# Performance work log

Measured on AMD Instinct MI355X. Metric: run time of the kernel, lower is better.

## Reference

```python
import jax, jax.numpy as jnp
import numpy as np

MAX_SLOTS = 8192


def _compress_lowest_importance_pair(x):
    """Vectorized version of the per-batch python loop: merge the adjacent pair
    with the lowest summed L2-norm into one averaged slot. [B,S,d] -> [B,S-1,d]."""
    B, S, d = x.shape
    imp = jnp.linalg.norm(x, axis=-1)              # [B, S]
    pair_scores = imp[:, :-1] + imp[:, 1:]          # [B, S-1]
    p = jnp.argmin(pair_scores, axis=1)             # [B] merge index per row
    idx = jnp.arange(S - 1)                         # output slot positions
    # gather: out[j] = x[j] for j<=p, x[j+1] for j>p
    g = idx[None, :] + (idx[None, :] > p[:, None]).astype(idx.dtype)  # [B, S-1]
    out = jnp.take_along_axis(x, g[:, :, None], axis=1)               # [B, S-1, d]
    left = jnp.take_along_axis(x, p[:, None, None], axis=1)           # [B, 1, d]
    right = jnp.take_along_axis(x, (p + 1)[:, None, None], axis=1)    # [B, 1, d]
    merged = 0.5 * (left + right)
    # overwrite position p with the merged slot
    out = jnp.where(idx[None, :, None] == p[:, None, None], merged, out)
    return out


def _compress_oldest_pair(x):
    merged = 0.5 * (x[:, :1, :] + x[:, 1:2, :])
    return jnp.concatenate([merged, x[:, 2:, :]], axis=1)


def setup_inputs() -> dict:
    key = jax.random.key(0)
    k1, k2 = jax.random.split(key)
    bank_states = jax.random.normal(k1, (16, 8192, 512), dtype=jnp.float32)
    refresh_states = jax.random.normal(k2, (16, 32, 512), dtype=jnp.float32)
    return {"bank_states": bank_states, "refresh_states": refresh_states}


def reference(bank_states, refresh_states):
    # write(): refresh_states.detach(); sizes here take the concat+compress path
    refresh = jax.lax.stop_gradient(refresh_states)
    updated = jnp.concatenate([bank_states, refresh], axis=1)  # [B, S_bank+S_ref, d]
    # shapes are static, so this python while unrolls a fixed number of steps
    while updated.shape[1] > MAX_SLOTS:
        if updated.shape[1] <= 2:
            updated = _compress_oldest_pair(updated)
        else:
            updated = _compress_lowest_importance_pair(updated)
    return updated
```

## Files before the change

### kernel.cpp

```cpp
#include <hip/hip_runtime.h>
#include <cstdint>
#include <cstddef>

#define B_DIM  16
#define S_BANK 8192
#define S_REF  32
#define S_TOT  8224
#define NMERGE 32
#define D      512
#define NCH    129

typedef float vfloat4 __attribute__((ext_vector_type(4)));
typedef unsigned long long u64;
#define DEADPK 0xFFFFFFFFFFFFFFFFULL

__device__ __forceinline__ int d_lo(double d){ union{double d; int i[2];}u; u.d=d; return u.i[0]; }
__device__ __forceinline__ int d_hi(double d){ union{double d; int i[2];}u; u.d=d; return u.i[1]; }
__device__ __forceinline__ double d_mk(int hi,int lo){ union{double d; int i[2];}u; u.i[0]=lo;u.i[1]=hi; return u.d; }
__device__ __forceinline__ int u_lo(u64 v){ return (int)(v & 0xFFFFFFFFULL); }
__device__ __forceinline__ int u_hi(u64 v){ return (int)(v >> 32); }
__device__ __forceinline__ u64 u_mk(int hi,int lo){ return ((u64)(unsigned)hi << 32) | (u64)(unsigned)lo; }
__device__ __forceinline__ u64 d_bits(double d){ union{double d; u64 u;}x; x.d=d; return x.u; }

__device__ __forceinline__ u64 pack_score(double s, int j) {
// ... 54 lines not shown
}
__device__ __forceinline__ double sum_wave(double v) {
    sum_level<0x111>(v); sum_level<0x112>(v); sum_level<0x114>(v);
    sum_level<0x118>(v); sum_level<0x142>(v); sum_level<0x143>(v);
    int lo = __builtin_amdgcn_readlane(d_lo(v), 63);
    int hi = __builtin_amdgcn_readlane(d_hi(v), 63);
    return d_mk(hi, lo);
}

__global__ __launch_bounds__(256) void norms_kernel(const float* __restrict__ bank,
                                                    const float* __restrict__ refresh,
                                                    double* __restrict__ norms) {
    int gw_lin = (int)((blockIdx.x * 256 + threadIdx.x) >> 6);
    int gw   = B_DIM * S_TOT - 1 - gw_lin;
    int lane = threadIdx.x & 63;
    int b = gw / S_TOT;
    int s = gw - b * S_TOT;
    const float4* src = (const float4*)(s < S_BANK
        ? bank    + ((size_t)b * S_BANK + s) * D
        : refresh + ((size_t)b * S_REF + (s - S_BANK)) * D);
    float4 f0 = src[lane];
    float4 f1 = src[lane + 64];
    double acc = 0.0;
    acc += (double)f0.x * f0.x + (double)f0.y * f0.y + (double)f0.z * f0.z + (double)f0.w * f0.w;
    acc += (double)f1.x * f1.x + (double)f1.y * f1.y + (double)f1.z * f1.z + (double)f1.w * f1.w;
    acc = sum_wave(acc);
    if (lane == 0) norms[gw] = sqrt(acc);
}

__global__ __launch_bounds__(256) void chunkmin_kernel(const double* __restrict__ norms,
                                                       u64* __restrict__ c_pk_g) {
    int w    = (int)((blockIdx.x * 256 + threadIdx.x) >> 6);
    int lane = threadIdx.x & 63;
    if (w >= B_DIM * NCH) return;
    int b = w / NCH;
    int c = w - b * NCH;
    int j = c * 64 + lane;
    u64 pk = DEADPK;
    if (j <= S_TOT - 2) {
        double a = norms[b * S_TOT + j];
        double d = norms[b * S_TOT + j + 1];
        pk = pack_score(a + d, j);
    }
    pk = lexmin_wave_u64(pk);
    if (lane == 0) c_pk_g[b * NCH + c] = pk;
}

__device__ __forceinline__ const float* slot_gptr(int id, int b,
        const float* bank, const float* refresh) {
    return (id < S_BANK) ? bank    + ((size_t)b * S_BANK + id) * D
                         : refresh + ((size_t)b * S_REF + (id - S_BANK)) * D;
}

struct FastLds {
    u64 pref[192];
    u64 suf[192];
};
struct FallLds {
    unsigned short s_next[S_TOT];
    float          s_mvec[NMERGE][D];
    unsigned short s_mpos[NMERGE];
    unsigned short s_dead[NMERGE];
};
union MergeLds { FastLds fast; FallLds fall; };

__global__ __launch_bounds__(256) void merge_kernel(const float* __restrict__ bank,
        const float* __restrict__ refresh, const double* __restrict__ norms,
        const u64* __restrict__ c_pk_g,
        float* __restrict__ merged, unsigned short* __restrict__ idx_out) {
    __shared__ double  s_imp[S_TOT];
    __shared__ u64     c_pk[NCH];
    __shared__ MergeLds u;
    __shared__ int     rec_L[NMERGE], rec_R[NMERGE];
    __shared__ u64     rec_chosen[NMERGE];
    __shared__ u64     s_PL, s_SR;
    __shared__ int     s_flag;

    const int t    = threadIdx.x;
    const int b    = blockIdx.x;
    const int lane = t & 63;
    const int wid  = t >> 6;
    const double INF = __builtin_inf();

    if (t < NCH) c_pk[t] = c_pk_g[b * NCH + t];
    __syncthreads();

    u64 pk_min0;
    {
        u64 a = c_pk[lane];
        u64 bq = c_pk[lane + 64];
        u64 c = (lane == 0) ? c_pk[128] : DEADPK;
        u64 m = (a < bq) ? a : bq;
        m = (m < c) ? m : c;
        pk_min0 = lexmin_wave_u64(m);
    }
    const int p0 = (int)(pk_min0 & 0x3FFFULL);

    const int cmid = p0 >> 6;
    int wsx = cmid - 1;
    if (wsx < 0) wsx = 0;
    if (wsx > NCH - 3) wsx = NCH - 3;
    const int ws  = wsx;
    const int wlo = ws * 64;

    float4 m0r, m1r;

    int do_fall = 1;
    {
        FastLds& F = u.fast;

        for (int j = t; j < 194; j += 256) {
            int g = wlo + j;
            if (g < S_TOT) s_imp[g] = norms[b * S_TOT + g];
        }
        __syncthreads();

        if (wid == 0) {
            const float4* gA = (const float4*)slot_gptr(p0, b, bank, refresh);
            const float4* gB = (const float4*)slot_gptr(p0 + 1, b, bank, refresh);
            float4 a0 = gA[2 * lane], a1 = gA[2 * lane + 1];
            float4 b0 = gB[2 * lane], b1 = gB[2 * lane + 1];
            int q;
            q = (p0 - 1 >= 0) ? p0 - 1 : 0;
            const float4* gq = (const float4*)slot_gptr(q, b, bank, refresh);
            float4 cL0 = gq[2 * lane], cL1 = gq[2 * lane + 1];
            q = (p0 + 2 <= S_TOT - 1) ? p0 + 2 : S_TOT - 1;
            gq = (const float4*)slot_gptr(q, b, bank, refresh);
            float4 cR0 = gq[2 * lane], cR1 = gq[2 * lane + 1];
            q = (p0 - 2 >= 0) ? p0 - 2 : 0;
            gq = (const float4*)slot_gptr(q, b, bank, refresh);
            float4 fL0 = gq[2 * lane], fL1 = gq[2 * lane + 1];
            q = (p0 + 3 <= S_TOT - 1) ? p0 + 3 : S_TOT - 1;
            gq = (const float4*)slot_gptr(q, b, bank, refresh);
            float4 fR0 = gq[2 * lane], fR1 = gq[2 * lane + 1];

            m0r.x = 0.5f * (a0.x + b0.x); m0r.y = 0.5f * (a0.y + b0.y);
            m0r.z = 0.5f * (a0.z + b0.z); m0r.w = 0.5f * (a0.w + b0.w);
            m1r.x = 0.5f * (a1.x + b1.x); m1r.y = 0.5f * (a1.y + b1.y);
            m1r.z = 0.5f * (a1.z + b1.z); m1r.w = 0.5f * (a1.w + b1.w);
            double ss = 0.0;
            ss += (double)m0r.x * m0r.x + (double)m0r.y * m0r.y + (double)m0r.z * m0r.z + (double)m0r.w * m0r.w;
            ss += (double)m1r.x * m1r.x + (double)m1r.y * m1r.y + (double)m1r.z * m1r.z + (double)m1r.w * m1r.w;
            double nrm = sqrt(sum_wave(ss));
            int L = p0, R = p0 + 1;
            if (t == 0) { rec_L[0] = L; rec_R[0] = R; rec_chosen[0] = pk_min0; }

            for (int step = 1; step < NMERGE; ++step) {
                const int cl = L - 1, cr = R + 1;
                const bool hasL = (cl >= 0);
                const bool hasR = (cr < S_TOT);
                const double il = hasL ? s_imp[cl] : INF;
                const double ir = hasR ? s_imp[cr] : INF;
                const u64 pkL = hasL ? pack_score(il + nrm, cl) : DEADPK;
                const u64 pkR = hasR ? pack_score(nrm + ir, L)  : DEADPK;
                const bool goL = (pkL < pkR);
                const u64 chosen = goL ? pkL : pkR;
                float4 a0s, a1s, b0s, b1s;
                if (goL) { a0s = cL0; a1s = cL1; b0s = m0r; b1s = m1r; }
                else     { a0s = m0r; a1s = m1r; b0s = cR0; b1s = cR1; }
                m0r.x = 0.5f * (a0s.x + b0s.x); m0r.y = 0.5f * (a0s.y + b0s.y);
                m0r.z = 0.5f * (a0s.z + b0s.z); m0r.w = 0.5f * (a0s.w + b0s.w);
                m1r.x = 0.5f * (a1s.x + b1s.x); m1r.y = 0.5f * (a1s.y + b1s.y);
                m1r.z = 0.5f * (a1s.z + b1s.z); m1r.w = 0.5f * (a1s.w + b1s.w);
                if (goL) {
                    L = cl;
                    cL0 = fL0; cL1 = fL1;
                    int nq = (L - 2 >= 0) ? L - 2 : 0;
                    const float4* gp = (const float4*)slot_gptr(nq, b, bank, refresh);
                    fL0 = gp[2 * lane]; fL1 = gp[2 * lane + 1];
                } else {
                    R = cr;
                    cR0 = fR0; cR1 = fR1;
                    int nq = (R + 2 <= S_TOT - 1) ? R + 2 : S_TOT - 1;
                    const float4* gp = (const float4*)slot_gptr(nq, b, bank, refresh);
                    fR0 = gp[2 * lane]; fR1 = gp[2 * lane + 1];
                }
                double ss2 = 0.0;
                ss2 += (double)m0r.x * m0r.x + (double)m0r.y * m0r.y + (double)m0r.z * m0r.z + (double)m0r.w * m0r.w;
                ss2 += (double)m1r.x * m1r.x + (double)m1r.y * m1r.y + (double)m1r.z * m1r.z + (double)m1r.w * m1r.w;
                nrm = sqrt(sum_wave(ss2));
                if (t == 0) { rec_L[step] = L; rec_R[step] = R; rec_chosen[step] = chosen; }
            }
        } else {
            int c = ws + (wid - 1);
            int idx = c * 64 + lane;
            u64 pk0 = (idx <= S_TOT - 2) ? pack_score(s_imp[idx] + s_imp[idx + 1], idx)
                                         : DEADPK;
            F.pref[idx - wlo] = scan_min_incl(pk0);
            F.suf[idx - wlo]  = scan_min_suffix(pk0, lane);
            if (wid == 1) {
                u64 x0 = (lane < ws) ? c_pk[lane] : DEADPK;
                u64 x1 = (lane + 64 < ws) ? c_pk[lane + 64] : DEADPK;
                u64 pl = (x0 < x1) ? x0 : x1;
                pl = lexmin_wave_u64(pl);
                if (lane == 0) s_PL = pl;
            }
            if (wid == 2) {
                u64 y0 = (lane > ws + 2) ? c_pk[lane] : DEADPK;
                u64 y1 = (lane + 64 > ws + 2) ? c_pk[lane + 64] : DEADPK;
                u64 y2 = (lane == 0 && 128 > ws + 2) ? c_pk[128] : DEADPK;
                u64 sr = (y0 < y1) ? y0 : y1;
                sr = (sr < y2) ? sr : y2;
                sr = lexmin_wave_u64(sr);
                if (lane == 0) s_SR = sr;
            }
        }
        __syncthreads();

        if (wid == 0) {
            u64 cf0 = F.pref[63], cf1 = F.pref[127];
            u64 sf1 = F.suf[64],  sf2 = F.suf[128];
            u64 PL = s_PL, SR = s_SR;
            bool ok = true;
            if (lane >= 1 && lane < NMERGE) {
                int Lp = rec_L[lane - 1], Rp = rec_R[lane - 1];
                int q1 = Lp - 2 - wlo;
                u64 ol = DEADPK;
                if (q1 >= 0) {
                    ol = F.pref[q1];
                    int r1 = q1 >> 6;
                    if (r1 >= 1 && cf0 < ol) ol = cf0;
                    if (r1 >= 2 && cf1 < ol) ol = cf1;
                }
                if (PL < ol) ol = PL;
                int q2 = Rp + 1 - wlo;
                u64 orr = F.suf[q2];
                int r2 = q2 >> 6;
                if (r2 <= 0 && sf1 < orr) orr = sf1;
                if (r2 <= 1 && sf2 < orr) orr = sf2;
                if (SR < orr) orr = SR;
                u64 O = (ol < orr) ? ol : orr;
                ok = rec_chosen[lane] < O;
            }
            if (lane == 0) ok = ok && (rec_R[NMERGE - 1] - rec_L[NMERGE - 1] == NMERGE);
            unsigned long long bad = __ballot(!ok);
            if (lane == 0) s_flag = (bad != 0ULL) ? 1 : 0;
        }
        __syncthreads();

        if (s_flag == 0) {
            if (wid == 0) {
                float4* dst = (float4*)(merged + ((size_t)b * NMERGE + (NMERGE - 1)) * D);
                dst[2 * lane] = m0r; dst[2 * lane + 1] = m1r;
            }
            const int Ls = rec_L[NMERGE - 1], Rs = rec_R[NMERGE - 1];
            for (int j = t; j < S_TOT; j += 256) {
                if (j < Ls)       idx_out[b * S_BANK + j] = (unsigned short)j;
                else if (j == Ls) idx_out[b * S_BANK + j] = (unsigned short)(S_TOT + NMERGE - 1);
                else if (j > Rs)  idx_out[b * S_BANK + j - NMERGE] = (unsigned short)j;
            }
            do_fall = 0;
        }
    }

    if (do_fall) {
        FallLds& G = u.fall;
        for (int j = t; j < S_TOT; j += 256)
            s_imp[j] = norms[b * S_TOT + j];
        for (int j = t; j < S_TOT; j += 256)
            G.s_next[j] = (unsigned short)((j + 1 < S_TOT) ? (j + 1) : 0xFFFF);
        __syncthreads();

        if (wid == 0) {
            u64 cv0 = c_pk[lane];
            u64 cv1 = c_pk[lane + 64];
            u64 cv2 = (lane == 0) ? c_pk[128] : DEADPK;

            int mpos_reg = -1;
            int prev_p = -1, prev_pv = -1, prev_nk = -1;
            int pvok = 0, nkok = 0;
            float4 mm0, mm1, pva0, pva1, pnk0, pnk1;

            for (int step = 0; step < NMERGE; ++step) {
                u64 m = (cv0 < cv1) ? cv0 : cv1;
                m = (m < cv2) ? m : cv2;
                m = lexmin_wave_u64(m);
                const int p = (int)(m & 0x3FFFULL);

                const bool hitA = pvok && (p == prev_pv);
                const bool hitB = nkok && (p == prev_p);

                int k, nk;
                float4 a0, a1, b0, b1;
                if (hitA) {
                    k = prev_p; nk = prev_nk;
                    a0 = pva0; a1 = pva1; b0 = mm0; b1 = mm1;
                } else if (hitB) {
                    k = prev_nk; nk = G.s_next[k];
                    a0 = mm0; a1 = mm1; b0 = pnk0; b1 = pnk1;
                } else {
                    k = G.s_next[p]; nk = G.s_next[k];
                    unsigned long long bA = __ballot((lane < step) && (mpos_reg == p));
                    const int ia = bA ? (S_TOT + 63 - __clzll(bA)) : p;
                    unsigned long long bB = __ballot((lane < step) && (mpos_reg == k));
                    const int ib = bB ? (S_TOT + 63 - __clzll(bB)) : k;
                    if (ia < S_TOT) { const float4* g = (const float4*)slot_gptr(ia, b, bank, refresh);
                                      a0 = g[2 * lane]; a1 = g[2 * lane + 1]; }
                    else            { const float4* g = (const float4*)&G.s_mvec[ia - S_TOT][0];
                                      a0 = g[2 * lane]; a1 = g[2 * lane + 1]; }
                    if (ib < S_TOT) { const float4* g = (const float4*)slot_gptr(ib, b, bank, refresh);
                                      b0 = g[2 * lane]; b1 = g[2 * lane + 1]; }
                    else            { const float4* g = (const float4*)&G.s_mvec[ib - S_TOT][0];
                                      b0 = g[2 * lane]; b1 = g[2 * lane + 1]; }
                }

                int pv;
                if (hitB) {
                    pv = prev_pv;
                } else {
                    int jq = p - 1 - lane;
                    bool plive = (jq >= 0) && (s_imp[jq] < 1e300);
                    unsigned long long pb = __ballot(plive);
                    pv = pb ? (p - __ffsll((unsigned long long)pb)) : -1;
                }

                const double imp_nk = s_imp[(nk != 0xFFFF) ? nk : 0];
                const double imp_pv = s_imp[(pv >= 0) ? pv : 0];
                const int chp = p >> 6, chk = k >> 6;
                const int chv = (pv >= 0) ? (pv >> 6) : -1;
                const int csB = (chk != chp) ? chk : -1;
                const int csC = (chv >= 0 && chv != chp && chv != chk) ? chv : -1;
                const int jjA = chp * 64 + lane;
                const bool validA = (jjA < S_TOT) && (jjA != k);
                const int rawNxtA = validA ? (int)G.s_next[jjA] : 0xFFFF;
                const double impA = validA ? s_imp[jjA] : INF;
                const int nxtA = (jjA == p) ? nk : rawNxtA;
                const double impNxtA = (nxtA != 0xFFFF) ? s_imp[nxtA] : INF;

                float4 m0, m1;
                m0.x = 0.5f * (a0.x + b0.x); m0.y = 0.5f * (a0.y + b0.y);
                m0.z = 0.5f * (a0.z + b0.z); m0.w = 0.5f * (a0.w + b0.w);
                m1.x = 0.5f * (a1.x + b1.x); m1.y = 0.5f * (a1.y + b1.y);
                m1.z = 0.5f * (a1.z + b1.z); m1.w = 0.5f * (a1.w + b1.w);
                {
                    float4* dst = (float4*)&G.s_mvec[step][0];
                    dst[2 * lane] = m0; dst[2 * lane + 1] = m1;
                }
                if (lane == step) mpos_reg = p;

                if (step + 1 < NMERGE) {
                    prev_p = p; prev_pv = pv; prev_nk = nk;
                    mm0 = m0; mm1 = m1;
                    pvok = (pv >= 0); nkok = (nk != 0xFFFF);
                    unsigned long long bpv = __ballot((lane <= step) && (mpos_reg == pv));
                    const int ipv = bpv ? (S_TOT + 63 - __clzll(bpv)) : pv;
                    unsigned long long bnk = __ballot((lane <= step) && (mpos_reg == nk));
                    const int ink = bnk ? (S_TOT + 63 - __clzll(bnk)) : nk;
                    if (pvok) {
                        if (ipv < S_TOT) { const float4* g = (const float4*)slot_gptr(ipv, b, bank, refresh);
                                           pva0 = g[2 * lane]; pva1 = g[2 * lane + 1]; }
                        else             { const float4* g = (const float4*)&G.s_mvec[ipv - S_TOT][0];
                                           pva0 = g[2 * lane]; pva1 = g[2 * lane + 1]; }
                    }
                    if (nkok) {
                        if (ink < S_TOT) { const float4* g = (const float4*)slot_gptr(ink, b, bank, refresh);
                                           pnk0 = g[2 * lane]; pnk1 = g[2 * lane + 1]; }
                        else             { const float4* g = (const float4*)&G.s_mvec[ink - S_TOT][0];
                                           pnk0 = g[2 * lane]; pnk1 = g[2 * lane + 1]; }
                    }
                }

                double ss = 0.0;
                ss += (double)m0.x * m0.x + (double)m0.y * m0.y + (double)m0.z * m0.z + (double)m0.w * m0.w;
                ss += (double)m1.x * m1.x + (double)m1.y * m1.y + (double)m1.z * m1.z + (double)m1.w * m1.w;
                const double nrm = sqrt(sum_wave(ss));

                if (lane == 0) {
                    G.s_next[p]    = (unsigned short)nk;
                    s_imp[k]       = INF;
                    s_imp[p]       = nrm;
                    G.s_mpos[step] = (unsigned short)p;
                    G.s_dead[step] = (unsigned short)k;
                }

                {
                    u64 sc = DEADPK;
                    if (validA && nxtA != 0xFFFF) {
                        double a0d = (jjA == p) ? nrm : impA;
                        if (a0d < 1e300) {
                            double a1d = (nxtA == p) ? nrm : impNxtA;
                            sc = pack_score(a0d + a1d, jjA);
                        }
                    }
                    sc = lexmin_wave_u64(sc);
                    if (chp < 64)       { if (lane == chp)      cv0 = sc; }
                    else if (chp < 128) { if (lane == chp - 64) cv1 = sc; }
                    else                { if (lane == 0)        cv2 = sc; }
                }
                if (csB >= 0) {
                    int jj = csB * 64 + lane;
                    u64 sc = DEADPK;
                    if (jj < S_TOT && jj != k) {
                        int nxt = (int)G.s_next[jj];
                        if (nxt != 0xFFFF) {
                            double a0d = s_imp[jj];
                            if (a0d < 1e300) sc = pack_score(a0d + s_imp[nxt], jj);
                        }
                    }
                    sc = lexmin_wave_u64(sc);
                    if (csB < 64)       { if (lane == csB)      cv0 = sc; }
                    else if (csB < 128) { if (lane == csB - 64) cv1 = sc; }
                    else                { if (lane == 0)        cv2 = sc; }
                }
                if (csC >= 0) {
                    int jj = csC * 64 + lane;
                    u64 sc = DEADPK;
                    if (jj < S_TOT && jj != k) {
                        int nxt = (int)G.s_next[jj];
                        if (nxt != 0xFFFF) {
                            double a0d = s_imp[jj];
                            if (a0d < 1e300) sc = pack_score(a0d + s_imp[nxt], jj);
                        }
                    }
                    sc = lexmin_wave_u64(sc);
                    if (csC < 64)       { if (lane == csC)      cv0 = sc; }
                    else if (csC < 128) { if (lane == csC - 64) cv1 = sc; }
                    else                { if (lane == 0)        cv2 = sc; }
                }
            }
        }
        __syncthreads();

        {
            const float4* src = (const float4*)&G.s_mvec[0][0];
            float4* dst = (float4*)(merged + (size_t)b * NMERGE * D);
            for (int i = t; i < NMERGE * D / 4; i += 256) dst[i] = src[i];
        }
        for (int j = t; j < S_TOT; j += 256) G.s_next[j] = 0xFFFF;
        __syncthreads();
        if (t == 0)
            for (int m2 = 0; m2 < NMERGE; ++m2) G.s_next[G.s_mpos[m2]] = (unsigned short)m2;
        __syncthreads();
        for (int j = t; j < S_TOT; j += 256) {
            if (s_imp[j] < 1e300) {
                int r = j;
                #pragma unroll
                for (int m2 = 0; m2 < NMERGE; ++m2) r -= (G.s_dead[m2] < j) ? 1 : 0;
                unsigned short lut = G.s_next[j];
                idx_out[b * S_BANK + r] = (lut != 0xFFFF) ? (unsigned short)(S_TOT + lut)
                                                          : (unsigned short)j;
            }
        }
    }
}

__global__ __launch_bounds__(256) void gather_kernel(const vfloat4* __restrict__ bank,
        const vfloat4* __restrict__ refresh, const vfloat4* __restrict__ merged,
        const unsigned short* __restrict__ idx, vfloat4* __restrict__ out) {
    size_t tid = (size_t)blockIdx.x * 256 + threadIdx.x;
    int slot = (int)(tid >> 7);
    int c    = (int)(tid & 127);
    int b    = slot >> 13;
    int src  = idx[slot];
    const vfloat4* sp;
    if (src < S_BANK)     sp = bank    + ((size_t)b * S_BANK + src) * (D / 4);
    else if (src < S_TOT) sp = refresh + ((size_t)b * S_REF + (src - S_BANK)) * (D / 4);
    else                  sp = merged  + ((size_t)b * NMERGE + (src - S_TOT)) * (D / 4);
    vfloat4 v = sp[c];
    __builtin_nontemporal_store(v, &out[tid]);
}

extern "C" void kernel_launch(void* const* d_in, const int* in_sizes, int n_in,
                              void* d_out, int out_size, void* d_ws, size_t ws_size,
                              hipStream_t stream) {
    const float* bank    = (const float*)d_in[0];
    const float* refresh = (const float*)d_in[1];

    double*         norms  = (double*)d_ws;
    float*          merged = (float*)((char*)d_ws + (size_t)B_DIM * S_TOT * sizeof(double));
    unsigned short* idx    = (unsigned short*)((char*)merged + (size_t)B_DIM * NMERGE * D * sizeof(float));
    u64*            c_pk_g = (u64*)((char*)idx + (size_t)B_DIM * S_BANK * sizeof(unsigned short));
    float*          out    = (float*)d_out;

    norms_kernel<<<(B_DIM * S_TOT) / 4, 256, 0, stream>>>(bank, refresh, norms);
    chunkmin_kernel<<<(B_DIM * NCH * 64 + 255) / 256, 256, 0, stream>>>(norms, c_pk_g);
    merge_kernel<<<B_DIM, 256, 0, stream>>>(bank, refresh, norms, c_pk_g, merged, idx);
    gather_kernel<<<(size_t)B_DIM * S_BANK * (D / 4) / 256, 256, 0, stream>>>(
        (const vfloat4*)bank, (const vfloat4*)refresh, (const vfloat4*)merged, idx, (vfloat4*)out);
}
```

Before: 144.9 us.

## Fuse merge and gather into one kernel with per-batch fallback kernel

Merges the greedy merge step and the output gather into one launch. Extra blocks copy the bulk rows, whose position is known from the first merge index p0, while 16 blocks run the local merge chain and write the window around p0 directly. This removes the idx indirection and the separate merged buffer. A flag per batch triggers a separate fallback kernel that recomputes everything for that batch when the local fast path fails verification. The cost is an extra launch and redundant work per bulk block, since each one recomputes p0 from the chunk minima.

```diff
diff --git a/kernel.cpp b/kernel.cpp
--- a/kernel.cpp
+++ b/kernel.cpp
@@ -130,35 +130,55 @@
                          : refresh + ((size_t)b * S_REF + (id - S_BANK)) * D;
 }
 
-struct FastLds {
-    u64 pref[192];
-    u64 suf[192];
-};
-struct FallLds {
-    unsigned short s_next[S_TOT];
-    float          s_mvec[NMERGE][D];
-    unsigned short s_mpos[NMERGE];
-    unsigned short s_dead[NMERGE];
-};
-union MergeLds { FastLds fast; FallLds fall; };
-
-__global__ __launch_bounds__(256) void merge_kernel(const float* __restrict__ bank,
+#define NBULK (B_DIM * 4096)
+
+__global__ __launch_bounds__(256) void fused_kernel(const float* __restrict__ bank,
         const float* __restrict__ refresh, const double* __restrict__ norms,
-        const u64* __restrict__ c_pk_g,
-        float* __restrict__ merged, unsigned short* __restrict__ idx_out) {
-    __shared__ double  s_imp[S_TOT];
-    __shared__ u64     c_pk[NCH];
-    __shared__ MergeLds u;
-    __shared__ int     rec_L[NMERGE], rec_R[NMERGE];
-    __shared__ u64     rec_chosen[NMERGE];
-    __shared__ u64     s_PL, s_SR;
-    __shared__ int     s_flag;
+        const u64* __restrict__ c_pk_g, int* __restrict__ flag_g,
+        vfloat4* __restrict__ out) {
+    __shared__ double s_wimp[194];
+    __shared__ u64    c_pk[NCH];
+    __shared__ u64    pref[192], suf[192];
+    __shared__ int    rec_L[NMERGE], rec_R[NMERGE];
+    __shared__ u64    rec_chosen[NMERGE];
+    __shared__ u64    s_PL, s_SR;
+    __shared__ int    s_flag;
+    __shared__ int    sh_p0;
 
     const int t    = threadIdx.x;
-    const int b    = blockIdx.x;
     const int lane = t & 63;
     const int wid  = t >> 6;
     const double INF = __builtin_inf();
+
+    if (blockIdx.x >= 16) {
+        int e  = blockIdx.x - 16;
+        int b  = e >> 12;
+        int pr = (e & 4095) << 1;
+        if (wid == 0) {
+            u64 a  = (lane < NCH) ? c_pk_g[b * NCH + lane] : DEADPK;
+            u64 b2 = (lane + 64 < NCH) ? c_pk_g[b * NCH + lane + 64] : DEADPK;
+            u64 m = (a < b2) ? a : b2;
+            u64 c2 = (lane == 0) ? c_pk_g[b * NCH + 128] : DEADPK;
+            m = (m < c2) ? m : c2;
+            m = lexmin_wave_u64(m);
+            if (lane == 0) sh_p0 = (int)(m & 0x3FFFULL);
+        }
+        __syncthreads();
+        const int p0 = sh_p0;
+        int r = pr + (t >> 7);
+        int c = t & 127;
+        int s = -1;
+        if (r < p0 - 31)      s = r;
+        else if (r > p0)      s = r + 32;
+        if (s >= 0) {
+            const vfloat4* sp = (const vfloat4*)slot_gptr(s, b, bank, refresh);
+            vfloat4 v = sp[c];
+            __builtin_nontemporal_store(v, &out[((size_t)b * S_BANK + r) * (D / 4) + c]);
+        }
+        return;
+    }
+
+    const int b = blockIdx.x;
 
     if (t < NCH) c_pk[t] = c_pk_g[b * NCH + t];
     __syncthreads();
@@ -181,361 +201,381 @@
     const int ws  = wsx;
     const int wlo = ws * 64;
 
+    for (int j = t; j < 194; j += 256) {
+        int g = wlo + j;
+        if (g < S_TOT) s_wimp[j] = norms[b * S_TOT + g];
+    }
+    __syncthreads();
+
     float4 m0r, m1r;
 
-    int do_fall = 1;
-    {
-        FastLds& F = u.fast;
-
-        for (int j = t; j < 194; j += 256) {
-            int g = wlo + j;
-            if (g < S_TOT) s_imp[g] = norms[b * S_TOT + g];
-        }
-        __syncthreads();
-
-        if (wid == 0) {
-            const float4* gA = (const float4*)slot_gptr(p0, b, bank, refresh);
-            const float4* gB = (const float4*)slot_gptr(p0 + 1, b, bank, refresh);
-            float4 a0 = gA[2 * lane], a1 = gA[2 * lane + 1];
-            float4 b0 = gB[2 * lane], b1 = gB[2 * lane + 1];
-            int q;
-            q = (p0 - 1 >= 0) ? p0 - 1 : 0;
-            const float4* gq = (const float4*)slot_gptr(q, b, bank, refresh);
-            float4 cL0 = gq[2 * lane], cL1 = gq[2 * lane + 1];
-            q = (p0 + 2 <= S_TOT - 1) ? p0 + 2 : S_TOT - 1;
-            gq = (const float4*)slot_gptr(q, b, bank, refresh);
-            float4 cR0 = gq[2 * lane], cR1 = gq[2 * lane + 1];
-            q = (p0 - 2 >= 0) ? p0 - 2 : 0;
-            gq = (const float4*)slot_gptr(q, b, bank, refresh);
-            float4 fL0 = gq[2 * lane], fL1 = gq[2 * lane + 1];
-            q = (p0 + 3 <= S_TOT - 1) ? p0 + 3 : S_TOT - 1;
-            gq = (const float4*)slot_gptr(q, b, bank, refresh);
-            float4 fR0 = gq[2 * lane], fR1 = gq[2 * lane + 1];
-
-            m0r.x = 0.5f * (a0.x + b0.x); m0r.y = 0.5f * (a0.y + b0.y);
-            m0r.z = 0.5f * (a0.z + b0.z); m0r.w = 0.5f * (a0.w + b0.w);
-            m1r.x = 0.5f * (a1.x + b1.x); m1r.y = 0.5f * (a1.y + b1.y);
-            m1r.z = 0.5f * (a1.z + b1.z); m1r.w = 0.5f * (a1.w + b1.w);
+    if (wid == 0) {
+        const float4* gA = (const float4*)slot_gptr(p0, b, bank, refresh);
+        const float4* gB = (const float4*)slot_gptr(p0 + 1, b, bank, refresh);
+        float4 a0 = gA[2 * lane], a1 = gA[2 * lane + 1];
+        float4 b0 = gB[2 * lane], b1 = gB[2 * lane + 1];
+        int q;
+        q = (p0 - 1 >= 0) ? p0 - 1 : 0;
+        const float4* gq = (const float4*)slot_gptr(q, b, bank, refresh);
+        float4 cL0 = gq[2 * lane], cL1 = gq[2 * lane + 1];
+        q = (p0 + 2 <= S_TOT - 1) ? p0 + 2 : S_TOT - 1;
+        gq = (const float4*)slot_gptr(q, b, bank, refresh);
+        float4 cR0 = gq[2 * lane], cR1 = gq[2 * lane + 1];
+        q = (p0 - 2 >= 0) ? p0 - 2 : 0;
+        gq = (const float4*)slot_gptr(q, b, bank, refresh);
+        float4 fL0 = gq[2 * lane], fL1 = gq[2 * lane + 1];
+        q = (p0 + 3 <= S_TOT - 1) ? p0 + 3 : S_TOT - 1;
+        gq = (const float4*)slot_gptr(q, b, bank, refresh);
+        float4 fR0 = gq[2 * lane], fR1 = gq[2 * lane + 1];
+
+        m0r.x = 0.5f * (a0.x + b0.x); m0r.y = 0.5f * (a0.y + b0.y);
+        m0r.z = 0.5f * (a0.z + b0.z); m0r.w = 0.5f * (a0.w + b0.w);
+        m1r.x = 0.5f * (a1.x + b1.x); m1r.y = 0.5f * (a1.y + b1.y);
+        m1r.z = 0.5f * (a1.z + b1.z); m1r.w = 0.5f * (a1.w + b1.w);
+        double ss = 0.0;
+        ss += (double)m0r.x * m0r.x + (double)m0r.y * m0r.y + (double)m0r.z * m0r.z + (double)m0r.w * m0r.w;
+        ss += (double)m1r.x * m1r.x + (double)m1r.y * m1r.y + (double)m1r.z * m1r.z + (double)m1r.w * m1r.w;
+        double nrm = sqrt(sum_wave(ss));
+        int L = p0, R = p0 + 1;
+        if (t == 0) { rec_L[0] = L; rec_R[0] = R; rec_chosen[0] = pk_min0; }
+
+        for (int step = 1; step < NMERGE; ++step) {
+            const int cl = L - 1, cr = R + 1;
+            const bool hasL = (cl >= 0);
+            const bool hasR = (cr < S_TOT);
+            const double il = hasL ? s_wimp[cl - wlo] : INF;
+            const double ir = hasR ? s_wimp[cr - wlo] : INF;
+            const u64 pkL = hasL ? pack_score(il + nrm, cl) : DEADPK;
+            const u64 pkR = hasR ? pack_score(nrm + ir, L)  : DEADPK;
+            const bool goL = (pkL < pkR);
+            const u64 chosen = goL ? pkL : pkR;
+            float4 a0s, a1s, b0s, b1s;
+            if (goL) { a0s = cL0; a1s = cL1; b0s = m0r; b1s = m1r; }
+            else     { a0s = m0r; a1s = m1r; b0s = cR0; b1s = cR1; }
+            m0r.x = 0.5f * (a0s.x + b0s.x); m0r.y = 0.5f * (a0s.y + b0s.y);
+            m0r.z = 0.5f * (a0s.z + b0s.z); m0r.w = 0.5f * (a0s.w + b0s.w);
+            m1r.x = 0.5f * (a1s.x + b1s.x); m1r.y = 0.5f * (a1s.y + b1s.y);
+            m1r.z = 0.5f * (a1s.z + b1s.z); m1r.w = 0.5f * (a1s.w + b1s.w);
+            if (goL) {
+                L = cl;
+                cL0 = fL0; cL1 = fL1;
+                int nq = (L - 2 >= 0) ? L - 2 : 0;
+                const float4* gp = (const float4*)slot_gptr(nq, b, bank, refresh);
+                fL0 = gp[2 * lane]; fL1 = gp[2 * lane + 1];
+            } else {
+                R = cr;
+                cR0 = fR0; cR1 = fR1;
+                int nq = (R + 2 <= S_TOT - 1) ? R + 2 : S_TOT - 1;
+                const float4* gp = (const float4*)slot_gptr(nq, b, bank, refresh);
+                fR0 = gp[2 * lane]; fR1 = gp[2 * lane + 1];
+            }
+            double ss2 = 0.0;
+            ss2 += (double)m0r.x * m0r.x + (double)m0r.y * m0r.y + (double)m0r.z * m0r.z + (double)m0r.w * m0r.w;
+            ss2 += (double)m1r.x * m1r.x + (double)m1r.y * m1r.y + (double)m1r.z * m1r.z + (double)m1r.w * m1r.w;
+            nrm = sqrt(sum_wave(ss2));
+            if (t == 0) { rec_L[step] = L; rec_R[step] = R; rec_chosen[step] = chosen; }
+        }
+    } else {
+        int c = ws + (wid - 1);
+        int idx = c * 64 + lane;
+        u64 pk0 = (idx <= S_TOT - 2)
+                    ? pack_score(s_wimp[idx - wlo] + s_wimp[idx + 1 - wlo], idx)
+                    : DEADPK;
+        pref[idx - wlo] = scan_min_incl(pk0);
+        suf[idx - wlo]  = scan_min_suffix(pk0, lane);
+        if (wid == 1) {
+            u64 x0 = (lane < ws) ? c_pk[lane] : DEADPK;
+            u64 x1 = (lane + 64 < ws) ? c_pk[lane + 64] : DEADPK;
+            u64 pl = (x0 < x1) ? x0 : x1;
+            pl = lexmin_wave_u64(pl);
+            if (lane == 0) s_PL = pl;
+        }
+        if (wid == 2) {
+            u64 y0 = (lane > ws + 2) ? c_pk[lane] : DEADPK;
+            u64 y1 = (lane + 64 > ws + 2) ? c_pk[lane + 64] : DEADPK;
+            u64 y2 = (lane == 0 && 128 > ws + 2) ? c_pk[128] : DEADPK;
+            u64 sr = (y0 < y1) ? y0 : y1;
+            sr = (sr < y2) ? sr : y2;
+            sr = lexmin_wave_u64(sr);
+            if (lane == 0) s_SR = sr;
+        }
+    }
+    __syncthreads();
+
+    if (wid == 0) {
+        u64 cf0 = pref[63], cf1 = pref[127];
+        u64 sf1 = suf[64],  sf2 = suf[128];
+        u64 PL = s_PL, SR = s_SR;
+        bool ok = true;
+        if (lane >= 1 && lane < NMERGE) {
+            int Lp = rec_L[lane - 1], Rp = rec_R[lane - 1];
+            int q1 = Lp - 2 - wlo;
+            u64 ol = DEADPK;
+            if (q1 >= 0) {
+                ol = pref[q1];
+                int r1 = q1 >> 6;
+                if (r1 >= 1 && cf0 < ol) ol = cf0;
+                if (r1 >= 2 && cf1 < ol) ol = cf1;
+            }
+            if (PL < ol) ol = PL;
+            int q2 = Rp + 1 - wlo;
+            u64 orr = suf[q2];
+            int r2 = q2 >> 6;
+            if (r2 <= 0 && sf1 < orr) orr = sf1;
+            if (r2 <= 1 && sf2 < orr) orr = sf2;
+            if (SR < orr) orr = SR;
+            u64 O = (ol < orr) ? ol : orr;
+            ok = rec_chosen[lane] < O;
+        }
+        if (lane == 0) ok = ok && (rec_R[NMERGE - 1] - rec_L[NMERGE - 1] == NMERGE);
+        unsigned long long bad = __ballot(!ok);
+        if (lane == 0) s_flag = (bad != 0ULL) ? 1 : 0;
+    }
+    __syncthreads();
+
+    if (t == 0) flag_g[b] = s_flag;
+    if (s_flag != 0) return;
+
+    const int Ls = rec_L[NMERGE - 1];
+    if (wid == 0) {
+        vfloat4 v0, v1;
+        v0.x = m0r.x; v0.y = m0r.y; v0.z = m0r.z; v0.w = m0r.w;
+        v1.x = m1r.x; v1.y = m1r.y; v1.z = m1r.z; v1.w = m1r.w;
+        __builtin_nontemporal_store(v0, &out[((size_t)b * S_BANK + Ls) * (D / 4) + 2 * lane]);
+        __builtin_nontemporal_store(v1, &out[((size_t)b * S_BANK + Ls) * (D / 4) + 2 * lane + 1]);
+    }
+    const int lo = (p0 - 31 > 0) ? p0 - 31 : 0;
+    const int hi = (p0 < S_BANK - 1) ? p0 : S_BANK - 1;
+    for (int r = lo + wid; r <= hi; r += 4) {
+        if (r == Ls) continue;
+        int s = (r < Ls) ? r : r + 32;
+        const vfloat4* sp = (const vfloat4*)slot_gptr(s, b, bank, refresh);
+        vfloat4 v0 = sp[2 * lane], v1 = sp[2 * lane + 1];
+        __builtin_nontemporal_store(v0, &out[((size_t)b * S_BANK + r) * (D / 4) + 2 * lane]);
+        __builtin_nontemporal_store(v1, &out[((size_t)b * S_BANK + r) * (D / 4) + 2 * lane + 1]);
+    }
+}
+
+struct FallLds {
+    unsigned short s_next[S_TOT];
+    float          s_mvec[NMERGE][D];
+    unsigned short s_mpos[NMERGE];
+    unsigned short s_dead[NMERGE];
+};
+
+__global__ __launch_bounds__(256) void fallback_kernel(const float* __restrict__ bank,
+        const float* __restrict__ refresh, const double* __restrict__ norms,
+        const u64* __restrict__ c_pk_g, const int* __restrict__ flag_g,
+        unsigned short* __restrict__ idx_out, vfloat4* __restrict__ out) {
+    const int b = blockIdx.x;
+    if (flag_g[b] == 0) return;
+
+    __shared__ double  s_imp[S_TOT];
+    __shared__ u64     c_pk[NCH];
+    __shared__ FallLds G;
+
+    const int t    = threadIdx.x;
+    const int lane = t & 63;
+    const int wid  = t >> 6;
+    const double INF = __builtin_inf();
+
+    if (t < NCH) c_pk[t] = c_pk_g[b * NCH + t];
+    for (int j = t; j < S_TOT; j += 256) {
+        s_imp[j] = norms[b * S_TOT + j];
+        G.s_next[j] = (unsigned short)((j + 1 < S_TOT) ? (j + 1) : 0xFFFF);
+    }
+    __syncthreads();
+
+    if (wid == 0) {
+        u64 cv0 = c_pk[lane];
+        u64 cv1 = c_pk[lane + 64];
+        u64 cv2 = (lane == 0) ? c_pk[128] : DEADPK;
+
+        int mpos_reg = -1;
+        int prev_p = -1, prev_pv = -1, prev_nk = -1;
+        int pvok = 0, nkok = 0;
+        float4 mm0, mm1, pva0, pva1, pnk0, pnk1;
+
+        for (int step = 0; step < NMERGE; ++step) {
+            u64 m = (cv0 < cv1) ? cv0 : cv1;
+            m = (m < cv2) ? m : cv2;
+            m = lexmin_wave_u64(m);
+            const int p = (int)(m & 0x3FFFULL);
+
+            const bool hitA = pvok && (p == prev_pv);
+            const bool hitB = nkok && (p == prev_p);
+
+            int k, nk;
+            float4 a0, a1, b0, b1;
+            if (hitA) {
+                k = prev_p; nk = prev_nk;
+                a0 = pva0; a1 = pva1; b0 = mm0; b1 = mm1;
+            } else if (hitB) {
+                k = prev_nk; nk = G.s_next[k];
+                a0 = mm0; a1 = mm1; b0 = pnk0; b1 = pnk1;
+            } else {
+                k = G.s_next[p]; nk = G.s_next[k];
+                unsigned long long bA = __ballot((lane < step) && (mpos_reg == p));
+                const int ia = bA ? (S_TOT + 63 - __clzll(bA)) : p;
+                unsigned long long bB = __ballot((lane < step) && (mpos_reg == k));
+                const int ib = bB ? (S_TOT + 63 - __clzll(bB)) : k;
+                if (ia < S_TOT) { const float4* g = (const float4*)slot_gptr(ia, b, bank, refresh);
+                                  a0 = g[2 * lane]; a1 = g[2 * lane + 1]; }
+                else            { const float4* g = (const float4*)&G.s_mvec[ia - S_TOT][0];
+                                  a0 = g[2 * lane]; a1 = g[2 * lane + 1]; }
+                if (ib < S_TOT) { const float4* g = (const float4*)slot_gptr(ib, b, bank, refresh);
+                                  b0 = g[2 * lane]; b1 = g[2 * lane + 1]; }
+                else            { const float4* g = (const float4*)&G.s_mvec[ib - S_TOT][0];
+                                  b0 = g[2 * lane]; b1 = g[2 * lane + 1]; }
+            }
+
+            int pv;
+            if (hitB) {
+                pv = prev_pv;
+            } else {
+                int jq = p - 1 - lane;
+                bool plive = (jq >= 0) && (s_imp[jq] < 1e300);
+                unsigned long long pb = __ballot(plive);
+                pv = pb ? (p - __ffsll((unsigned long long)pb)) : -1;
+            }
+
+            const double imp_nk = s_imp[(nk != 0xFFFF) ? nk : 0];
+            const double imp_pv = s_imp[(pv >= 0) ? pv : 0];
+            const int chp = p >> 6, chk = k >> 6;
+            const int chv = (pv >= 0) ? (pv >> 6) : -1;
+            const int csB = (chk != chp) ? chk : -1;
+            const int csC = (chv >= 0 && chv != chp && chv != chk) ? chv : -1;
+            const int jjA = chp * 64 + lane;
+            const bool validA = (jjA < S_TOT) && (jjA != k);
+            const int rawNxtA = validA ? (int)G.s_next[jjA] : 0xFFFF;
+            const double impA = validA ? s_imp[jjA] : INF;
+            const int nxtA = (jjA == p) ? nk : rawNxtA;
+            const double impNxtA = (nxtA != 0xFFFF) ? s_imp[nxtA] : INF;
+
+            float4 m0, m1;
+            m0.x = 0.5f * (a0.x + b0.x); m0.y = 0.5f * (a0.y + b0.y);
+            m0.z = 0.5f * (a0.z + b0.z); m0.w = 0.5f * (a0.w + b0.w);
+            m1.x = 0.5f * (a1.x + b1.x); m1.y = 0.5f * (a1.y + b1.y);
+            m1.z = 0.5f * (a1.z + b1.z); m1.w = 0.5f * (a1.w + b1.w);
+            {
+                float4* dst = (float4*)&G.s_mvec[step][0];
+                dst[2 * lane] = m0; dst[2 * lane + 1] = m1;
+            }
+            if (lane == step) mpos_reg = p;
+
+            if (step + 1 < NMERGE) {
+                prev_p = p; prev_pv = pv; prev_nk = nk;
+                mm0 = m0; mm1 = m1;
+                pvok = (pv >= 0); nkok = (nk != 0xFFFF);
+                unsigned long long bpv = __ballot((lane <= step) && (mpos_reg == pv));
+                const int ipv = bpv ? (S_TOT + 63 - __clzll(bpv)) : pv;
+                unsigned long long bnk = __ballot((lane <= step) && (mpos_reg == nk));
+                const int ink = bnk ? (S_TOT + 63 - __clzll(bnk)) : nk;
+                if (pvok) {
+                    if (ipv < S_TOT) { const float4* g = (const float4*)slot_gptr(ipv, b, bank, refresh);
+                                       pva0 = g[2 * lane]; pva1 = g[2 * lane + 1]; }
+                    else             { const float4* g = (const float4*)&G.s_mvec[ipv - S_TOT][0];
+                                       pva0 = g[2 * lane]; pva1 = g[2 * lane + 1]; }
+                }
+                if (nkok) {
+                    if (ink < S_TOT) { const float4* g = (const float4*)slot_gptr(ink, b, bank, refresh);
+                                       pnk0 = g[2 * lane]; pnk1 = g[2 * lane + 1]; }
+                    else             { const float4* g = (const float4*)&G.s_mvec[ink - S_TOT][0];
+                                       pnk0 = g[2 * lane]; pnk1 = g[2 * lane + 1]; }
+                }
+            }
+
             double ss = 0.0;
-            ss += (double)m0r.x * m0r.x + (double)m0r.y * m0r.y + (double)m0r.z * m0r.z + (double)m0r.w * m0r.w;
-            ss += (double)m1r.x * m1r.x + (double)m1r.y * m1r.y + (double)m1r.z * m1r.z + (double)m1r.w * m1r.w;
-            double nrm = sqrt(sum_wave(ss));
-            int L = p0, R = p0 + 1;
-            if (t == 0) { rec_L[0] = L; rec_R[0] = R; rec_chosen[0] = pk_min0; }
-
-            for (int step = 1; step < NMERGE; ++step) {
-                const int cl = L - 1, cr = R + 1;
-                const bool hasL = (cl >= 0);
-                const bool hasR = (cr < S_TOT);
-                const double il = hasL ? s_imp[cl] : INF;
-                const double ir = hasR ? s_imp[cr] : INF;
-                const u64 pkL = hasL ? pack_score(il + nrm, cl) : DEADPK;
-                const u64 pkR = hasR ? pack_score(nrm + ir, L)  : DEADPK;
-                const bool goL = (pkL < pkR);
-                const u64 chosen = goL ? pkL : pkR;
-                float4 a0s, a1s, b0s, b1s;
-                if (goL) { a0s = cL0; a1s = cL1; b0s = m0r; b1s = m1r; }
-                else     { a0s = m0r; a1s = m1r; b0s = cR0; b1s = cR1; }
-                m0r.x = 0.5f * (a0s.x + b0s.x); m0r.y = 0.5f * (a0s.y + b0s.y);
-                m0r.z = 0.5f * (a0s.z + b0s.z); m0r.w = 0.5f * (a0s.w + b0s.w);
-                m1r.x = 0.5f * (a1s.x + b1s.x); m1r.y = 0.5f * (a1s.y + b1s.y);
-                m1r.z = 0.5f * (a1s.z + b1s.z); m1r.w = 0.5f * (a1s.w + b1s.w);
-                if (goL) {
-                    L = cl;
-                    cL0 = fL0; cL1 = fL1;
-                    int nq = (L - 2 >= 0) ? L - 2 : 0;
-                    const float4* gp = (const float4*)slot_gptr(nq, b, bank, refresh);
-                    fL0 = gp[2 * lane]; fL1 = gp[2 * lane + 1];
-                } else {
-                    R = cr;
-                    cR0 = fR0; cR1 = fR1;
-                    int nq = (R + 2 <= S_TOT - 1) ? R + 2 : S_TOT - 1;
-                    const float4* gp = (const float4*)slot_gptr(nq, b, bank, refresh);
-                    fR0 = gp[2 * lane]; fR1 = gp[2 * lane + 1];
-                }
-                double ss2 = 0.0;
-                ss2 += (double)m0r.x * m0r.x + (double)m0r.y * m0r.y + (double)m0r.z * m0r.z + (double)m0r.w * m0r.w;
-                ss2 += (double)m1r.x * m1r.x + (double)m1r.y * m1r.y + (double)m1r.z * m1r.z + (double)m1r.w * m1r.w;
-                nrm = sqrt(sum_wave(ss2));
-                if (t == 0) { rec_L[step] = L; rec_R[step] = R; rec_chosen[step] = chosen; }
-            }
-        } else {
-            int c = ws + (wid - 1);
-            int idx = c * 64 + lane;
-            u64 pk0 = (idx <= S_TOT - 2) ? pack_score(s_imp[idx] + s_imp[idx + 1], idx)
-                                         : DEADPK;
-            F.pref[idx - wlo] = scan_min_incl(pk0);
-            F.suf[idx - wlo]  = scan_min_suffix(pk0, lane);
-            if (wid == 1) {
-                u64 x0 = (lane < ws) ? c_pk[lane] : DEADPK;
-                u64 x1 = (lane + 64 < ws) ? c_pk[lane + 64] : DEADPK;
-                u64 pl = (x0 < x1) ? x0 : x1;
-                pl = lexmin_wave_u64(pl);
-                if (lane == 0) s_PL = pl;
-            }
-            if (wid == 2) {
-                u64 y0 = (lane > ws + 2) ? c_pk[lane] : DEADPK;
-                u64 y1 = (lane + 64 > ws + 2) ? c_pk[lane + 64] : DEADPK;
-                u64 y2 = (lane == 0 && 128 > ws + 2) ? c_pk[128] : DEADPK;
-                u64 sr = (y0 < y1) ? y0 : y1;
-                sr = (sr < y2) ? sr : y2;
-                sr = lexmin_wave_u64(sr);
-                if (lane == 0) s_SR = sr;
-            }
-        }
-        __syncthreads();
-
-        if (wid == 0) {
-            u64 cf0 = F.pref[63], cf1 = F.pref[127];
-            u64 sf1 = F.suf[64],  sf2 = F.suf[128];
-            u64 PL = s_PL, SR = s_SR;
-            bool ok = true;
-            if (lane >= 1 && lane < NMERGE) {
-                int Lp = rec_L[lane - 1], Rp = rec_R[lane - 1];
-                int q1 = Lp - 2 - wlo;
-                u64 ol = DEADPK;
-                if (q1 >= 0) {
-                    ol = F.pref[q1];
-                    int r1 = q1 >> 6;
-                    if (r1 >= 1 && cf0 < ol) ol = cf0;
-                    if (r1 >= 2 && cf1 < ol) ol = cf1;
-                }
-                if (PL < ol) ol = PL;
-                int q2 = Rp + 1 - wlo;
-                u64 orr = F.suf[q2];
-                int r2 = q2 >> 6;
-                if (r2 <= 0 && sf1 < orr) orr = sf1;
-                if (r2 <= 1 && sf2 < orr) orr = sf2;
-                if (SR < orr) orr = SR;
-                u64 O = (ol < orr) ? ol : orr;
-                ok = rec_chosen[lane] < O;
-            }
-            if (lane == 0) ok = ok && (rec_R[NMERGE - 1] - rec_L[NMERGE - 1] == NMERGE);
-            unsigned long long bad = __ballot(!ok);
-            if (lane == 0) s_flag = (bad != 0ULL) ? 1 : 0;
-        }
-        __syncthreads();
-
-        if (s_flag == 0) {
-            if (wid == 0) {
-                float4* dst = (float4*)(merged + ((size_t)b * NMERGE + (NMERGE - 1)) * D);
-                dst[2 * lane] = m0r; dst[2 * lane + 1] = m1r;
-            }
-            const int Ls = rec_L[NMERGE - 1], Rs = rec_R[NMERGE - 1];
-            for (int j = t; j < S_TOT; j += 256) {
-                if (j < Ls)       idx_out[b * S_BANK + j] = (unsigned short)j;
-                else if (j == Ls) idx_out[b * S_BANK + j] = (unsigned short)(S_TOT + NMERGE - 1);
-                else if (j > Rs)  idx_out[b * S_BANK + j - NMERGE] = (unsigned short)j;
-            }
-            do_fall = 0;
-        }
-    }
-
-    if (do_fall) {
-        FallLds& G = u.fall;
-        for (int j = t; j < S_TOT; j += 256)
-            s_imp[j] = norms[b * S_TOT + j];
-        for (int j = t; j < S_TOT; j += 256)
-            G.s_next[j] = (unsigned short)((j + 1 < S_TOT) ? (j + 1) : 0xFFFF);
-        __syncthreads();
-
-        if (wid == 0) {
-            u64 cv0 = c_pk[lane];
-            u64 cv1 = c_pk[lane + 64];
-            u64 cv2 = (lane == 0) ? c_pk[128] : DEADPK;
-
-            int mpos_reg = -1;
-            int prev_p = -1, prev_pv = -1, prev_nk = -1;
-            int pvok = 0, nkok = 0;
-            float4 mm0, mm1, pva0, pva1, pnk0, pnk1;
-
-            for (int step = 0; step < NMERGE; ++step) {
-                u64 m = (cv0 < cv1) ? cv0 : cv1;
-                m = (m < cv2) ? m : cv2;
-                m = lexmin_wave_u64(m);
-                const int p = (int)(m & 0x3FFFULL);
-
-                const bool hitA = pvok && (p == prev_pv);
-                const bool hitB = nkok && (p == prev_p);
-
-                int k, nk;
-                float4 a0, a1, b0, b1;
-                if (hitA) {
-                    k = prev_p; nk = prev_nk;
-                    a0 = pva0; a1 = pva1; b0 = mm0; b1 = mm1;
-                } else if (hitB) {
-                    k = prev_nk; nk = G.s_next[k];
-                    a0 = mm0; a1 = mm1; b0 = pnk0; b1 = pnk1;
-                } else {
-                    k = G.s_next[p]; nk = G.s_next[k];
-                    unsigned long long bA = __ballot((lane < step) && (mpos_reg == p));
-                    const int ia = bA ? (S_TOT + 63 - __clzll(bA)) : p;
-                    unsigned long long bB = __ballot((lane < step) && (mpos_reg == k));
-                    const int ib = bB ? (S_TOT + 63 - __clzll(bB)) : k;
-                    if (ia < S_TOT) { const float4* g = (const float4*)slot_gptr(ia, b, bank, refresh);
-                                      a0 = g[2 * lane]; a1 = g[2 * lane + 1]; }
-                    else            { const float4* g = (const float4*)&G.s_mvec[ia - S_TOT][0];
-                                      a0 = g[2 * lane]; a1 = g[2 * lane + 1]; }
-                    if (ib < S_TOT) { const float4* g = (const float4*)slot_gptr(ib, b, bank, refresh);
-                                      b0 = g[2 * lane]; b1 = g[2 * lane + 1]; }
-                    else            { const float4* g = (const float4*)&G.s_mvec[ib - S_TOT][0];
-                                      b0 = g[2 * lane]; b1 = g[2 * lane + 1]; }
-                }
-
-                int pv;
-                if (hitB) {
-                    pv = prev_pv;
-                } else {
-                    int jq = p - 1 - lane;
-                    bool plive = (jq >= 0) && (s_imp[jq] < 1e300);
-                    unsigned long long pb = __ballot(plive);
-                    pv = pb ? (p - __ffsll((unsigned long long)pb)) : -1;
-                }
-
-                const double imp_nk = s_imp[(nk != 0xFFFF) ? nk : 0];
-                const double imp_pv = s_imp[(pv >= 0) ? pv : 0];
-                const int chp = p >> 6, chk = k >> 6;
-                const int chv = (pv >= 0) ? (pv >> 6) : -1;
-                const int csB = (chk != chp) ? chk : -1;
-                const int csC = (chv >= 0 && chv != chp && chv != chk) ? chv : -1;
-                const int jjA = chp * 64 + lane;
-                const bool validA = (jjA < S_TOT) && (jjA != k);
-                const int rawNxtA = validA ? (int)G.s_next[jjA] : 0xFFFF;
-                const double impA = validA ? s_imp[jjA] : INF;
-                const int nxtA = (jjA == p) ? nk : rawNxtA;
-                const double impNxtA = (nxtA != 0xFFFF) ? s_imp[nxtA] : INF;
-
-                float4 m0, m1;
-                m0.x = 0.5f * (a0.x + b0.x); m0.y = 0.5f * (a0.y + b0.y);
-                m0.z = 0.5f * (a0.z + b0.z); m0.w = 0.5f * (a0.w + b0.w);
-                m1.x = 0.5f * (a1.x + b1.x); m1.y = 0.5f * (a1.y + b1.y);
-                m1.z = 0.5f * (a1.z + b1.z); m1.w = 0.5f * (a1.w + b1.w);
-                {
-                    float4* dst = (float4*)&G.s_mvec[step][0];
-                    dst[2 * lane] = m0; dst[2 * lane + 1] = m1;
-                }
-                if (lane == step) mpos_reg = p;
-
-                if (step + 1 < NMERGE) {
-                    prev_p = p; prev_pv = pv; prev_nk = nk;
-                    mm0 = m0; mm1 = m1;
-                    pvok = (pv >= 0); nkok = (nk != 0xFFFF);
-                    unsigned long long bpv = __ballot((lane <= step) && (mpos_reg == pv));
-                    const int ipv = bpv ? (S_TOT + 63 - __clzll(bpv)) : pv;
-                    unsigned long long bnk = __ballot((lane <= step) && (mpos_reg == nk));
-                    const int ink = bnk ? (S_TOT + 63 - __clzll(bnk)) : nk;
-                    if (pvok) {
-                        if (ipv < S_TOT) { const float4* g = (const float4*)slot_gptr(ipv, b, bank, refresh);
-                                           pva0 = g[2 * lane]; pva1 = g[2 * lane + 1]; }
-                        else             { const float4* g = (const float4*)&G.s_mvec[ipv - S_TOT][0];
-                                           pva0 = g[2 * lane]; pva1 = g[2 * lane + 1]; }
-                    }
-                    if (nkok) {
-                        if (ink < S_TOT) { const float4* g = (const float4*)slot_gptr(ink, b, bank, refresh);
-                                           pnk0 = g[2 * lane]; pnk1 = g[2 * lane + 1]; }
-                        else             { const float4* g = (const float4*)&G.s_mvec[ink - S_TOT][0];
-                                           pnk0 = g[2 * lane]; pnk1 = g[2 * lane + 1]; }
+            ss += (double)m0.x * m0.x + (double)m0.y * m0.y + (double)m0.z * m0.z + (double)m0.w * m0.w;
+            ss += (double)m1.x * m1.x + (double)m1.y * m1.y + (double)m1.z * m1.z + (double)m1.w * m1.w;
+            const double nrm = sqrt(sum_wave(ss));
+
+            if (lane == 0) {
+                G.s_next[p]    = (unsigned short)nk;
+                s_imp[k]       = INF;
+                s_imp[p]       = nrm;
+                G.s_mpos[step] = (unsigned short)p;
+                G.s_dead[step] = (unsigned short)k;
+            }
+
+            {
+                u64 sc = DEADPK;
+                if (validA && nxtA != 0xFFFF) {
+                    double a0d = (jjA == p) ? nrm : impA;
+                    if (a0d < 1e300) {
+                        double a1d = (nxtA == p) ? nrm : impNxtA;
+                        sc = pack_score(a0d + a1d, jjA);
                     }
                 }
-
-                double ss = 0.0;
-                ss += (double)m0.x * m0.x + (double)m0.y * m0.y + (double)m0.z * m0.z + (double)m0.w * m0.w;
-                ss += (double)m1.x * m1.x + (double)m1.y * m1.y + (double)m1.z * m1.z + (double)m1.w * m1.w;
-                const double nrm = sqrt(sum_wave(ss));
-
-                if (lane == 0) {
-                    G.s_next[p]    = (unsigned short)nk;
-                    s_imp[k]       = INF;
-                    s_imp[p]       = nrm;
-                    G.s_mpos[step] = (unsigned short)p;
-                    G.s_dead[step] = (unsigned short)k;
+                sc = lexmin_wave_u64(sc);
+                if (chp < 64)       { if (lane == chp)      cv0 = sc; }
+                else if (chp < 128) { if (lane == chp - 64) cv1 = sc; }
+                else                { if (lane == 0)        cv2 = sc; }
+            }
+            if (csB >= 0) {
+                int jj = csB * 64 + lane;
+                u64 sc = DEADPK;
+                if (jj < S_TOT && jj != k) {
+                    int nxt = (int)G.s_next[jj];
+                    if (nxt != 0xFFFF) {
+                        double a0d = s_imp[jj];
+                        if (a0d < 1e300) sc = pack_score(a0d + s_imp[nxt], jj);
+                    }
                 }
-
-                {
-                    u64 sc = DEADPK;
-                    if (validA && nxtA != 0xFFFF) {
-                        double a0d = (jjA == p) ? nrm : impA;
-                        if (a0d < 1e300) {
-                            double a1d = (nxtA == p) ? nrm : impNxtA;
-                            sc = pack_score(a0d + a1d, jjA);
-                        }
+                sc = lexmin_wave_u64(sc);
+                if (csB < 64)       { if (lane == csB)      cv0 = sc; }
+                else if (csB < 128) { if (lane == csB - 64) cv1 = sc; }
+                else                { if (lane == 0)        cv2 = sc; }
+            }
+            if (csC >= 0) {
+                int jj = csC * 64 + lane;
+                u64 sc = DEADPK;
+                if (jj < S_TOT && jj != k) {
+                    int nxt = (int)G.s_next[jj];
+                    if (nxt != 0xFFFF) {
+                        double a0d = s_imp[jj];
+                        if (a0d < 1e300) sc = pack_score(a0d + s_imp[nxt], jj);
                     }
-                    sc = lexmin_wave_u64(sc);
-                    if (chp < 64)       { if (lane == chp)      cv0 = sc; }
-                    else if (chp < 128) { if (lane == chp - 64) cv1 = sc; }
-                    else                { if (lane == 0)        cv2 = sc; }
                 }
-                if (csB >= 0) {
-                    int jj = csB * 64 + lane;
-                    u64 sc = DEADPK;
-                    if (jj < S_TOT && jj != k) {
-                        int nxt = (int)G.s_next[jj];
-                        if (nxt != 0xFFFF) {
-                            double a0d = s_imp[jj];
-                            if (a0d < 1e300) sc = pack_score(a0d + s_imp[nxt], jj);
-                        }
-                    }
-                    sc = lexmin_wave_u64(sc);
-                    if (csB < 64)       { if (lane == csB)      cv0 = sc; }
-                    else if (csB < 128) { if (lane == csB - 64) cv1 = sc; }
-                    else                { if (lane == 0)        cv2 = sc; }
-                }
-                if (csC >= 0) {
-                    int jj = csC * 64 + lane;
-                    u64 sc = DEADPK;
-                    if (jj < S_TOT && jj != k) {
-                        int nxt = (int)G.s_next[jj];
-                        if (nxt != 0xFFFF) {
-                            double a0d = s_imp[jj];
-                            if (a0d < 1e300) sc = pack_score(a0d + s_imp[nxt], jj);
-                        }
-                    }
-                    sc = lexmin_wave_u64(sc);
-                    if (csC < 64)       { if (lane == csC)      cv0 = sc; }
-                    else if (csC < 128) { if (lane == csC - 64) cv1 = sc; }
-                    else                { if (lane == 0)        cv2 = sc; }
-                }
-            }
-        }
-        __syncthreads();
-
-        {
-            const float4* src = (const float4*)&G.s_mvec[0][0];
-            float4* dst = (float4*)(merged + (size_t)b * NMERGE * D);
-            for (int i = t; i < NMERGE * D / 4; i += 256) dst[i] = src[i];
-        }
-        for (int j = t; j < S_TOT; j += 256) G.s_next[j] = 0xFFFF;
-        __syncthreads();
-        if (t == 0)
-            for (int m2 = 0; m2 < NMERGE; ++m2) G.s_next[G.s_mpos[m2]] = (unsigned short)m2;
-        __syncthreads();
-        for (int j = t; j < S_TOT; j += 256) {
-            if (s_imp[j] < 1e300) {
-                int r = j;
-                #pragma unroll
-                for (int m2 = 0; m2 < NMERGE; ++m2) r -= (G.s_dead[m2] < j) ? 1 : 0;
-                unsigned short lut = G.s_next[j];
-                idx_out[b * S_BANK + r] = (lut != 0xFFFF) ? (unsigned short)(S_TOT + lut)
-                                                          : (unsigned short)j;
-            }
-        }
-    }
-}
-
-__global__ __launch_bounds__(256) void gather_kernel(const vfloat4* __restrict__ bank,
-        const vfloat4* __restrict__ refresh, const vfloat4* __restrict__ merged,
-        const unsigned short* __restrict__ idx, vfloat4* __restrict__ out) {
-    size_t tid = (size_t)blockIdx.x * 256 + threadIdx.x;
-    int slot = (int)(tid >> 7);
-    int c    = (int)(tid & 127);
-    int b    = slot >> 13;
-    int src  = idx[slot];
-    const vfloat4* sp;
-    if (src < S_BANK)     sp = bank    + ((size_t)b * S_BANK + src) * (D / 4);
-    else if (src < S_TOT) sp = refresh + ((size_t)b * S_REF + (src - S_BANK)) * (D / 4);
-    else                  sp = merged  + ((size_t)b * NMERGE + (src - S_TOT)) * (D / 4);
-    vfloat4 v = sp[c];
-    __builtin_nontemporal_store(v, &out[tid]);
+                sc = lexmin_wave_u64(sc);
+                if (csC < 64)       { if (lane == csC)      cv0 = sc; }
+                else if (csC < 128) { if (lane == csC - 64) cv1 = sc; }
+                else                { if (lane == 0)        cv2 = sc; }
+            }
+        }
+    }
+    __syncthreads();
+
+    for (int j = t; j < S_TOT; j += 256) G.s_next[j] = 0xFFFF;
+    __syncthreads();
+    if (t == 0)
+        for (int m2 = 0; m2 < NMERGE; ++m2) G.s_next[G.s_mpos[m2]] = (unsigned short)m2;
+    __syncthreads();
+    for (int j = t; j < S_TOT; j += 256) {
+        if (s_imp[j] < 1e300) {
+            int r = j;
+            #pragma unroll
+            for (int m2 = 0; m2 < NMERGE; ++m2) r -= (G.s_dead[m2] < j) ? 1 : 0;
+            unsigned short lut = G.s_next[j];
+            idx_out[b * S_BANK + r] = (lut != 0xFFFF) ? (unsigned short)(S_TOT + lut)
+                                                      : (unsigned short)j;
+        }
+    }
+    __syncthreads();
+
+    for (int w = t; w < S_BANK * (D / 4); w += 256) {
+        int r = w >> 7, c = w & 127;
+        int src = idx_out[b * S_BANK + r];
+        vfloat4 v;
+        if (src < S_TOT) {
+            const vfloat4* sp = (const vfloat4*)slot_gptr(src, b, bank, refresh);
+            v = sp[c];
+        } else {
+            const vfloat4* sp = (const vfloat4*)&G.s_mvec[src - S_TOT][0];
+            v = sp[c];
+        }
+        __builtin_nontemporal_store(v, &out[((size_t)b * S_BANK + r) * (D / 4) + c]);
+    }
 }
 
 extern "C" void kernel_launch(void* const* d_in, const int* in_sizes, int n_in,
@@ -545,14 +585,13 @@
     const float* refresh = (const float*)d_in[1];
 
     double*         norms  = (double*)d_ws;
-    float*          merged = (float*)((char*)d_ws + (size_t)B_DIM * S_TOT * sizeof(double));
-    unsigned short* idx    = (unsigned short*)((char*)merged + (size_t)B_DIM * NMERGE * D * sizeof(float));
-    u64*            c_pk_g = (u64*)((char*)idx + (size_t)B_DIM * S_BANK * sizeof(unsigned short));
-    float*          out    = (float*)d_out;
+    u64*            c_pk_g = (u64*)((char*)d_ws + (size_t)B_DIM * S_TOT * sizeof(double));
+    int*            flag_g = (int*)((char*)c_pk_g + (size_t)B_DIM * NCH * sizeof(u64));
+    unsigned short* idx    = (unsigned short*)((char*)flag_g + 64 * sizeof(int));
+    vfloat4*        out    = (vfloat4*)d_out;
 
     norms_kernel<<<(B_DIM * S_TOT) / 4, 256, 0, stream>>>(bank, refresh, norms);
     chunkmin_kernel<<<(B_DIM * NCH * 64 + 255) / 256, 256, 0, stream>>>(norms, c_pk_g);
-    merge_kernel<<<B_DIM, 256, 0, stream>>>(bank, refresh, norms, c_pk_g, merged, idx);
-    gather_kernel<<<(size_t)B_DIM * S_BANK * (D / 4) / 256, 256, 0, stream>>>(
-        (const vfloat4*)bank, (const vfloat4*)refresh, (const vfloat4*)merged, idx, (vfloat4*)out);
-}
+    fused_kernel<<<16 + NBULK, 256, 0, stream>>>(bank, refresh, norms, c_pk_g, flag_g, out);
+    fallback_kernel<<<B_DIM, 256, 0, stream>>>(bank, refresh, norms, c_pk_g, flag_g, idx, out);
+}
```

New measurement: 131.2 us. -9.5%, faster.
